# Optimization experiments

Hardware: AMD Instinct MI355X
Metric: run time of the kernel (lower is better)

The kernel has to match this reference:

```python
import jax, jax.numpy as jnp
import numpy as np

D_MODEL = 1024
NUM_HEADS = 16
D_K = D_MODEL // NUM_HEADS


def setup_inputs() -> dict:
    key = jax.random.key(0)
    ks = jax.random.split(key, 9)
    s = 1.0 / np.sqrt(D_MODEL)
    x = jax.random.normal(ks[0], (2, 2048, D_MODEL), dtype=jnp.float32)
    mk = lambda k: jax.random.uniform(k, (D_MODEL, D_MODEL), jnp.float32, -s, s)
    mb = lambda k: jax.random.uniform(k, (D_MODEL,), jnp.float32, -s, s)
    return {
        "x": x,
        "Wq": mk(ks[1]), "bq": mb(ks[2]),
        "Wk": mk(ks[3]), "bk": mb(ks[4]),
        "Wv": mk(ks[5]), "bv": mb(ks[6]),
        "Wo": mk(ks[7]), "bo": mb(ks[8]),
    }


def _attn(x, Wq, bq, Wk, bk, Wv, bv, Wo, bo):
    B, S, _ = x.shape
    # torch Linear: y = x @ W.T + b; weights stored [out, in]
    def proj(W, b):
        y = jnp.einsum('bsd,ed->bse', x, W) + b
        return y.reshape(B, S, NUM_HEADS, D_K).transpose(0, 2, 1, 3)  # [B,H,S,Dk]
    Q = proj(Wq, bq)
    K = proj(Wk, bk)
    V = proj(Wv, bv)
    scale = 1.0 / np.sqrt(D_K).astype(np.float32)
    scores = jnp.einsum('bhqd,bhkd->bhqk', Q, K) * scale  # [B,H,S,S]
    # FAITHFUL to source: softmax over dim=1 (the HEAD axis), a quirk of the original code
    attn = jax.nn.softmax(scores, axis=1)
    context = jnp.einsum('bhqk,bhkd->bhqd', attn, V)  # [B,H,S,Dk]
    context = context.transpose(0, 2, 1, 3).reshape(B, S, D_MODEL)
    return jnp.einsum('bsd,ed->bse', context, Wo) + bo


def reference(x, Wq, bq, Wk, bk, Wv, bv, Wo, bo):
    return _attn(x, Wq, bq, Wk, bk, Wv, bv, Wo, bo)
```

## Files before the change

### kernel.cpp

```cpp
#include <hip/hip_runtime.h>


#define D_MODEL 1024
#define NH 16
#define DKH 64
#define SEQ 2048
#define NB 2
#define NTOK (NB * SEQ)
#define OSC 0.180336880f

typedef float f32x4 __attribute__((ext_vector_type(4)));
typedef short bf16x8 __attribute__((ext_vector_type(8)));

static __device__ __forceinline__ unsigned short f2bf(float x) {
    union { float f; unsigned int u; } c; c.f = x;
    unsigned int r = (c.u + 0x7FFFu + ((c.u >> 16) & 1u)) >> 16;
    return (unsigned short)r;
}
static __device__ __forceinline__ unsigned int pack2(float a, float b) {
    return (unsigned int)f2bf(a) | ((unsigned int)f2bf(b) << 16);
}
static __device__ __forceinline__ unsigned int pack2rn(float a, float b) {
    union { float f; unsigned int u; } ca, cb; ca.f = a; cb.f = b;
    return __builtin_amdgcn_perm(cb.u + 0x8000u, ca.u + 0x8000u, 0x07060302u);
}
static __device__ __forceinline__ unsigned int pack2tr(float a, float b) {
    union { float f; unsigned int u; } ca, cb; ca.f = a; cb.f = b;
    return __builtin_amdgcn_perm(cb.u, ca.u, 0x07060302u);
}
static __device__ __forceinline__ float bflo(unsigned int u) {
    union { unsigned int x; float f; } c; c.x = u << 16; return c.f;
}
static __device__ __forceinline__ float bfhi(unsigned int u) {
    union { unsigned int x; float f; } c; c.x = u & 0xFFFF0000u; return c.f;
}
static __device__ __forceinline__ f32x4 mfma16(uint4 a, uint4 b, f32x4 c) {
    return __builtin_amdgcn_mfma_f32_16x16x32_bf16(
        __builtin_bit_cast(bf16x8, a), __builtin_bit_cast(bf16x8, b), c, 0, 0, 0);
}
static __device__ __forceinline__ void gl_lds16(const unsigned short* g, unsigned short* l) {
    __builtin_amdgcn_global_load_lds(
        (const __attribute__((address_space(1))) unsigned int*)g,
        (__attribute__((address_space(3))) unsigned int*)l, 16, 0, 0);
}
static __device__ __forceinline__ int fsw(int row) {
    return (row & 7) ^ ((row >> 2) & 7);
}

__global__ __launch_bounds__(256) void cvt_k(const float* __restrict__ x,
                                             unsigned short* __restrict__ xb)
{
    size_t i = ((size_t)blockIdx.x * 256 + threadIdx.x) * 8;
    float4 a = *(const float4*)(x + i);
    float4 b = *(const float4*)(x + i + 4);
    uint4 p = { pack2(a.x, a.y), pack2(a.z, a.w), pack2(b.x, b.y), pack2(b.z, b.w) };
    *(uint4*)(xb + i) = p;
}

__global__ __launch_bounds__(256) void cvt_w3(
    const float* __restrict__ w0, const float* __restrict__ w1,
    const float* __restrict__ w2, unsigned short* __restrict__ outb)
{
    int sel = blockIdx.x >> 9;
    int blk = blockIdx.x & 511;
    const float* src = (sel == 0) ? w0 : (sel == 1) ? w1 : w2;
    size_t i = ((size_t)blk * 256 + threadIdx.x) * 8;
    float4 a = *(const float4*)(src + i);
    float4 b = *(const float4*)(src + i + 4);
    uint4 p = { pack2(a.x, a.y), pack2(a.z, a.w), pack2(b.x, b.y), pack2(b.z, b.w) };
    *(uint4*)(outb + (size_t)sel * D_MODEL * D_MODEL + i) = p;
}

__global__ __launch_bounds__(256) void gemm_qkv3(
    const unsigned short* __restrict__ A, const unsigned short* __restrict__ Wb3,
    const float* __restrict__ bq, const float* __restrict__ bk,
    const float* __restrict__ bv, unsigned short* __restrict__ Qh,
    unsigned short* __restrict__ Kh, unsigned short* __restrict__ Vt)
{
    __shared__ unsigned short lds[16384];
    unsigned short* lA = lds;
    unsigned short* lB = lds + 8192;
    const int tid = threadIdx.x;
    const int wv = tid >> 6, lane = tid & 63, quad = lane >> 4, lm = lane & 15;
    const int sel = blockIdx.x >> 3;
    const int m0 = blockIdx.y * 128, n0 = (blockIdx.x & 7) * 128;
    const int sub = lane >> 3, chl = (lane & 7) ^ sub;
    const unsigned short* Wb = Wb3 + (size_t)sel * D_MODEL * D_MODEL;
    const float* bias = (sel == 0) ? bq : (sel == 1) ? bk : bv;
    const float osc = (sel == 0) ? OSC : 1.0f;

    f32x4 acc[2][8] = {};

    for (int k0 = 0; k0 < D_MODEL; k0 += 64) {
        __syncthreads();
#pragma unroll
        for (int j = 0; j < 4; ++j) {
            int rbase = wv * 32 + j * 8;
            gl_lds16(A + (size_t)(m0 + rbase + sub) * D_MODEL + k0 + chl * 8,
                     &lA[rbase * 64]);
            gl_lds16(Wb + (size_t)(n0 + rbase + sub) * D_MODEL + k0 + chl * 8,
                     &lB[rbase * 64]);
        }
        __syncthreads();
#pragma unroll
        for (int ks = 0; ks < 2; ++ks) {
            uint4 af[2];
#pragma unroll
            for (int mt = 0; mt < 2; ++mt)
                af[mt] = *(const uint4*)&lA[(wv * 32 + mt * 16 + lm) * 64 +
                                            ((ks * 4 + quad) ^ (lm & 7)) * 8];
#pragma unroll
            for (int nt = 0; nt < 8; ++nt) {
                uint4 bf = *(const uint4*)&lB[(nt * 16 + lm) * 64 +
                                              ((ks * 4 + quad) ^ (lm & 7)) * 8];
                acc[0][nt] = mfma16(af[0], bf, acc[0][nt]);
                acc[1][nt] = mfma16(af[1], bf, acc[1][nt]);
            }
        }
    }

    if (sel < 2) {
        unsigned short* out = (sel == 0) ? Qh : Kh;
#pragma unroll
        for (int nt = 0; nt < 8; ++nt) {
            int n = n0 + nt * 16 + lm;
            float bvv = bias[n];
            int h = n >> 6, d = n & 63;
#pragma unroll
            for (int mt = 0; mt < 2; ++mt)
#pragma unroll
                for (int r = 0; r < 4; ++r) {
                    int m = m0 + wv * 32 + mt * 16 + quad * 4 + r;
                    int b = m >> 11, q = m & 2047;
                    out[((size_t)(b * NH + h) * SEQ + q) * DKH + d] =
                        f2bf((acc[mt][nt][r] + bvv) * osc);
                }
        }
    } else {
        __syncthreads();
        unsigned short* T = lds;
#pragma unroll
        for (int nt = 0; nt < 8; ++nt) {
            float bvv = bias[n0 + nt * 16 + lm];
            int nl = nt * 16 + lm;
#pragma unroll
            for (int mt = 0; mt < 2; ++mt) {
                int ml = wv * 32 + mt * 16 + quad * 4;
                uint2 p = { pack2rn(acc[mt][nt][0] + bvv, acc[mt][nt][1] + bvv),
                            pack2rn(acc[mt][nt][2] + bvv, acc[mt][nt][3] + bvv) };
                *(uint2*)&T[nl * 128 + ml] = p;
            }
        }
        __syncthreads();
        int row = tid >> 1, seg = tid & 1;
        int b = m0 >> 11, s0 = m0 & 2047;
        unsigned short* dst = Vt + ((size_t)(b * D_MODEL) + n0 + row) * SEQ + s0 + seg * 64;
        const unsigned short* src = &T[row * 128 + seg * 64];
#pragma unroll
        for (int i = 0; i < 8; ++i)
            *(uint4*)(dst + i * 8) = *(const uint4*)(src + i * 8);
    }
}

template <int KS>
__global__ __launch_bounds__(256) void psum(const unsigned short* __restrict__ OP,
                                            unsigned short* __restrict__ OPs)
{
    const size_t M = (size_t)NTOK * D_MODEL;
    size_t i = ((size_t)blockIdx.x * 256 + threadIdx.x) * 8;
    uint4 a = *(const uint4*)(OP + i);
    float lo0 = bflo(a.x), hi0 = bfhi(a.x), lo1 = bflo(a.y), hi1 = bfhi(a.y);
    float lo2 = bflo(a.z), hi2 = bfhi(a.z), lo3 = bflo(a.w), hi3 = bfhi(a.w);
#pragma unroll
    for (int p = 1; p < KS; ++p) {
        uint4 u = *(const uint4*)(OP + p * M + i);
        lo0 += bflo(u.x); hi0 += bfhi(u.x); lo1 += bflo(u.y); hi1 += bfhi(u.y);
        lo2 += bflo(u.z); hi2 += bfhi(u.z); lo3 += bflo(u.w); hi3 += bfhi(u.w);
    }
    uint4 o = { pack2(lo0, hi0), pack2(lo1, hi1), pack2(lo2, hi2), pack2(lo3, hi3) };
    *(uint4*)(OPs + i) = o;
}

__global__ __launch_bounds__(256) void gemm_osum1(
    const unsigned short* __restrict__ OPs, const unsigned short* __restrict__ WoB,
    const float* __restrict__ bias, float* __restrict__ out)
{
    __shared__ unsigned short lds[16384];
    unsigned short* lA = lds;
    unsigned short* lB = lds + 8192;
    const int tid = threadIdx.x;
    const int wv = tid >> 6, lane = tid & 63, quad = lane >> 4, lm = lane & 15;
    const int m0 = blockIdx.y * 128, n0 = blockIdx.x * 128;
    const int sub = lane >> 3, chl = (lane & 7) ^ sub;
    const int b = m0 >> 11, q0 = m0 & 2047;

    f32x4 acc[2][8] = {};

    for (int k0 = 0; k0 < D_MODEL; k0 += 64) {
        const int h = k0 >> 6;
        const unsigned short* Ab = OPs + ((size_t)(b * NH + h) * SEQ + q0) * DKH;
        __syncthreads();
#pragma unroll
        for (int j = 0; j < 4; ++j) {
            int rbase = wv * 32 + j * 8;
            gl_lds16(Ab + (size_t)(rbase + sub) * DKH + chl * 8, &lA[rbase * 64]);
            gl_lds16(WoB + (size_t)(n0 + rbase + sub) * D_MODEL + k0 + chl * 8,
                     &lB[rbase * 64]);
        }
        __syncthreads();
#pragma unroll
        for (int ks = 0; ks < 2; ++ks) {
            uint4 af[2];
#pragma unroll
            for (int mt = 0; mt < 2; ++mt)
                af[mt] = *(const uint4*)&lA[(wv * 32 + mt * 16 + lm) * 64 +
                                            ((ks * 4 + quad) ^ (lm & 7)) * 8];
#pragma unroll
            for (int nt = 0; nt < 8; ++nt) {
                uint4 bf = *(const uint4*)&lB[(nt * 16 + lm) * 64 +
                                              ((ks * 4 + quad) ^ (lm & 7)) * 8];
                acc[0][nt] = mfma16(af[0], bf, acc[0][nt]);
                acc[1][nt] = mfma16(af[1], bf, acc[1][nt]);
            }
        }
    }
#pragma unroll
    for (int nt = 0; nt < 8; ++nt) {
        int n = n0 + nt * 16 + lm;
        float bv = bias[n];
#pragma unroll
        for (int mt = 0; mt < 2; ++mt)
#pragma unroll
            for (int r = 0; r < 4; ++r) {
                int m = m0 + wv * 32 + mt * 16 + quad * 4 + r;
                out[(size_t)m * D_MODEL + n] = acc[mt][nt][r] + bv;
            }
    }
}

__global__ __launch_bounds__(256) void zker2(
    const unsigned short* __restrict__ Qh, const unsigned short* __restrict__ Kh,
    unsigned short* __restrict__ rz)
{
    __shared__ unsigned short lK[128 * 64];
    const int tid = threadIdx.x;
    const int wv = tid >> 6, lane = tid & 63, quad = lane >> 4, lm = lane & 15;
    const int lid = blockIdx.x;
    const int xcd = lid & 7, slot = lid >> 3;
    const int qb = slot & 15, col = xcd * 4 + (slot >> 4);
    const int b = col >> 4, kb = col & 15;
    const int q0 = qb * 128, k0 = kb * 128;
    const int srow = tid >> 3, sc = tid & 7;

    f32x4 z[2][8] = {};

    for (int h = 0; h < NH; ++h) {
        const size_t kbase = ((size_t)(b * NH + h) * SEQ + k0) * DKH;
        __syncthreads();
#pragma unroll
        for (int j = 0; j < 4; ++j) {
            int row = j * 32 + srow;
            int g = sc ^ fsw(row);
            gl_lds16(Kh + kbase + (size_t)row * 64 + g * 8, &lK[(j * 32 + wv * 8) * 64]);
        }
        uint4 bq[2][2];
#pragma unroll
        for (int qs = 0; qs < 2; ++qs) {
            const unsigned short* qp = Qh +
                ((size_t)(b * NH + h) * SEQ + q0 + wv * 32 + qs * 16 + lm) * DKH + quad * 8;
            bq[qs][0] = *(const uint4*)qp;
            bq[qs][1] = *(const uint4*)(qp + 32);
        }
        __syncthreads();
#pragma unroll
        for (int kt = 0; kt < 8; ++kt) {
            int krow = kt * 16 + lm;
            uint4 a0 = *(const uint4*)&lK[krow * 64 + ((quad) ^ fsw(krow)) * 8];
            uint4 a1 = *(const uint4*)&lK[krow * 64 + ((4 + quad) ^ fsw(krow)) * 8];
#pragma unroll
            for (int qs = 0; qs < 2; ++qs) {
                f32x4 sf = {0.f, 0.f, 0.f, 0.f};
                sf = mfma16(a0, bq[qs][0], sf);
                sf = mfma16(a1, bq[qs][1], sf);
#pragma unroll
                for (int r = 0; r < 4; ++r)
                    z[qs][kt][r] += __builtin_amdgcn_exp2f(sf[r]);
            }
        }
    }
#pragma unroll
    for (int qs = 0; qs < 2; ++qs) {
        int q = q0 + wv * 32 + qs * 16 + lm;
#pragma unroll
        for (int kt = 0; kt < 8; ++kt) {
            int k = k0 + kt * 16 + quad * 4;
            float l0 = __builtin_amdgcn_logf(z[qs][kt][0]);
            float l1 = __builtin_amdgcn_logf(z[qs][kt][1]);
            float l2 = __builtin_amdgcn_logf(z[qs][kt][2]);
            float l3 = __builtin_amdgcn_logf(z[qs][kt][3]);
            uint2 st = { pack2rn(-l0, -l1), pack2rn(-l2, -l3) };
            *(uint2*)(rz + (size_t)(b * SEQ + q) * SEQ + k) = st;
        }
    }
}

template <int KS>
__global__ __launch_bounds__(256) void attn4(
    const unsigned short* __restrict__ Qh, const unsigned short* __restrict__ Kh,
    const unsigned short* __restrict__ Vt, const unsigned short* __restrict__ rz,
    unsigned short* __restrict__ OP)
{
    __shared__ unsigned short lK[64 * 64];
    __shared__ unsigned short lV[64 * 64];
    const int tid = threadIdx.x;
    const int wv = tid >> 6, lane = tid & 63, quad = lane >> 4, lm = lane & 15;
    const int lid = blockIdx.x;
    const int xcd = lid & 7, slot = lid >> 3;
    const int qb = slot & 15;
    const int combo = xcd * (4 * KS) + (slot >> 4);
    const int bh = combo / KS, ksl = combo % KS;
    const int b = bh >> 4, h = bh & 15;
    const int q0 = qb * 128;
    const int NIT = (SEQ / KS) / 64;
    const int kbeg = ksl * (SEQ / KS);
    const int q0w = q0 + wv * 32;
    const size_t hb = (size_t)(b * NH + h) * SEQ;
    const int srow = tid >> 3, sc = tid & 7;

    uint4 qf[2][2];
#pragma unroll
    for (int qs = 0; qs < 2; ++qs)
#pragma unroll
        for (int ks = 0; ks < 2; ++ks)
            qf[qs][ks] = *(const uint4*)(Qh + (hb + q0w + qs * 16 + lm) * DKH +
                                         ks * 32 + quad * 8);

    const int perm = ((lm >> 2) * 8) + (lm & 3);
    f32x4 oa[4][2] = {};

    for (int kt = 0; kt < NIT; ++kt) {
        const int kbase = kbeg + kt * 64;
        __syncthreads();
#pragma unroll
        for (int j = 0; j < 2; ++j) {
            int row = j * 32 + srow;
            int g = sc ^ fsw(row);
            gl_lds16(Kh + (hb + kbase + row) * DKH + g * 8,
                     &lK[(j * 32 + wv * 8) * 64]);
        }
#pragma unroll
        for (int j = 0; j < 2; ++j) {
            int row = j * 32 + srow;
            int g = sc ^ fsw(row);
            gl_lds16(Vt + ((size_t)(b * D_MODEL) + h * DKH + row) * SEQ + kbase + g * 8,
                     &lV[(j * 32 + wv * 8) * 64]);
        }
        uint4 rv[2][2];
#pragma unroll
        for (int qs = 0; qs < 2; ++qs)
#pragma unroll
            for (int gr = 0; gr < 2; ++gr)
                rv[gr][qs] = *(const uint4*)(rz +
                    (size_t)(b * SEQ + q0w + qs * 16 + lm) * SEQ +
                    kbase + gr * 32 + quad * 8);
        __syncthreads();

#pragma unroll
        for (int gr = 0; gr < 2; ++gr) {
            f32x4 sf[2][2];
#pragma unroll
            for (int qs = 0; qs < 2; ++qs) {
                uint4 rq = rv[gr][qs];
                sf[0][qs][0] = bflo(rq.x); sf[0][qs][1] = bfhi(rq.x);
                sf[0][qs][2] = bflo(rq.y); sf[0][qs][3] = bfhi(rq.y);
                sf[1][qs][0] = bflo(rq.z); sf[1][qs][1] = bfhi(rq.z);
                sf[1][qs][2] = bflo(rq.w); sf[1][qs][3] = bfhi(rq.w);
            }
#pragma unroll
            for (int sel = 0; sel < 2; ++sel) {
                int key = gr * 32 + perm + sel * 4;
#pragma unroll
                for (int ks = 0; ks < 2; ++ks) {
                    uint4 kfv = *(const uint4*)&lK[key * 64 +
                                                   ((ks * 4 + quad) ^ fsw(key)) * 8];
                    sf[sel][0] = mfma16(kfv, qf[0][ks], sf[sel][0]);
                    sf[sel][1] = mfma16(kfv, qf[1][ks], sf[sel][1]);
                }
            }
            uint4 pk[2];
#pragma unroll
            for (int qs = 0; qs < 2; ++qs) {
                float p00 = __builtin_amdgcn_exp2f(sf[0][qs][0]);
                float p01 = __builtin_amdgcn_exp2f(sf[0][qs][1]);
                float p02 = __builtin_amdgcn_exp2f(sf[0][qs][2]);
                float p03 = __builtin_amdgcn_exp2f(sf[0][qs][3]);
                float p10 = __builtin_amdgcn_exp2f(sf[1][qs][0]);
                float p11 = __builtin_amdgcn_exp2f(sf[1][qs][1]);
                float p12 = __builtin_amdgcn_exp2f(sf[1][qs][2]);
                float p13 = __builtin_amdgcn_exp2f(sf[1][qs][3]);
                pk[qs].x = pack2tr(p00, p01);
                pk[qs].y = pack2tr(p02, p03);
                pk[qs].z = pack2tr(p10, p11);
                pk[qs].w = pack2tr(p12, p13);
            }
#pragma unroll
            for (int ct = 0; ct < 4; ++ct) {
                int vrow = ct * 16 + lm;
                uint4 vfv = *(const uint4*)&lV[vrow * 64 +
                                               ((gr * 4 + quad) ^ fsw(vrow)) * 8];
                oa[ct][0] = mfma16(vfv, pk[0], oa[ct][0]);
                oa[ct][1] = mfma16(vfv, pk[1], oa[ct][1]);
            }
        }
    }

    unsigned short* op = OP + (size_t)ksl * NTOK * D_MODEL;
#pragma unroll
    for (int ct = 0; ct < 4; ++ct)
#pragma unroll
        for (int qs = 0; qs < 2; ++qs) {
            uint2 st = { pack2rn(oa[ct][qs][0], oa[ct][qs][1]),
                         pack2rn(oa[ct][qs][2], oa[ct][qs][3]) };
            *(uint2*)(op + (hb + q0w + qs * 16 + lm) * DKH + ct * 16 + quad * 4) = st;
        }
}

extern "C" void kernel_launch(void* const* d_in, const int* in_sizes, int n_in,
                              void* d_out, int out_size, void* d_ws, size_t ws_size,
                              hipStream_t stream)
{
    const float* x  = (const float*)d_in[0];
    const float* Wq = (const float*)d_in[1];
    const float* bq = (const float*)d_in[2];
    const float* Wk = (const float*)d_in[3];
    const float* bk = (const float*)d_in[4];
    const float* Wv = (const float*)d_in[5];
    const float* bv = (const float*)d_in[6];
    const float* Wo = (const float*)d_in[7];
    const float* bo = (const float*)d_in[8];
    float* out = (float*)d_out;

    const size_t M  = (size_t)NTOK * D_MODEL;
    const size_t RZ = (size_t)NB * SEQ * SEQ;
    unsigned short* ws = (unsigned short*)d_ws;
    unsigned short* rzb = ws;
    unsigned short* xb  = ws;
    unsigned short* Qh  = ws + RZ;
    unsigned short* Kh  = Qh + M;
    unsigned short* Vt  = Kh + M;
    unsigned short* OP  = Vt + M;
    unsigned short* Wb3 = OP;
    unsigned short* OPs = Qh;
    unsigned short* WoB = rzb;

    const size_t need4 = (RZ + 3 * M + 4 * M) * sizeof(unsigned short);
    const size_t need2 = (RZ + 3 * M + 2 * M) * sizeof(unsigned short);
    const int KS = (ws_size >= need4) ? 4 : (ws_size >= need2) ? 2 : 1;

    cvt_k<<<2048, 256, 0, stream>>>(x, xb);
    cvt_w3<<<1536, 256, 0, stream>>>(Wq, Wk, Wv, Wb3);
    gemm_qkv3<<<dim3(24, 32), 256, 0, stream>>>(xb, Wb3, bq, bk, bv, Qh, Kh, Vt);
    zker2<<<512, 256, 0, stream>>>(Qh, Kh, rzb);
    if (KS == 4)      attn4<4><<<2048, 256, 0, stream>>>(Qh, Kh, Vt, rzb, OP);
    else if (KS == 2) attn4<2><<<1024, 256, 0, stream>>>(Qh, Kh, Vt, rzb, OP);
    else              attn4<1><<<512, 256, 0, stream>>>(Qh, Kh, Vt, rzb, OP);
    cvt_k<<<512, 256, 0, stream>>>(Wo, WoB);
    if (KS == 4)      psum<4><<<2048, 256, 0, stream>>>(OP, OPs);
    else if (KS == 2) psum<2><<<2048, 256, 0, stream>>>(OP, OPs);
    else              OPs = OP;
    gemm_osum1<<<dim3(8, 32), 256, 0, stream>>>(OPs, WoB, bo, out);
}
```

Baseline: 268.6 us.

## Double-buffer K/V LDS staging and prefetch next tile in score and attention kernels

Both the log-normaliser kernel (zker2) and the attention kernel (attn4) now use two LDS buffers. The next head's or next key tile's K/V is issued into the alternate buffer before computing on the current one, and the Q fragments and rz rows are prefetched into registers the same way. This leaves one barrier per iteration instead of two and is meant to hide global-load latency behind the MFMA and exp work. s_setprio is raised around the MFMA sequences to favour matrix issue. The cost is doubled LDS per block and extra live registers for the prefetched fragments, which may lower occupancy.

```diff
diff --git a/kernel.cpp b/kernel.cpp
--- a/kernel.cpp
+++ b/kernel.cpp
@@ -242,7 +242,7 @@
     const unsigned short* __restrict__ Qh, const unsigned short* __restrict__ Kh,
     unsigned short* __restrict__ rz)
 {
-    __shared__ unsigned short lK[128 * 64];
+    __shared__ unsigned short lK[2][128 * 64];
     const int tid = threadIdx.x;
     const int wv = tid >> 6, lane = tid & 63, quad = lane >> 4, lm = lane & 15;
     const int lid = blockIdx.x;
@@ -254,37 +254,62 @@
 
     f32x4 z[2][8] = {};
 
-    for (int h = 0; h < NH; ++h) {
-        const size_t kbase = ((size_t)(b * NH + h) * SEQ + k0) * DKH;
-        __syncthreads();
+    auto stagek = [&](int buf, int hh) {
+        const size_t kbase = ((size_t)(b * NH + hh) * SEQ + k0) * DKH;
 #pragma unroll
         for (int j = 0; j < 4; ++j) {
             int row = j * 32 + srow;
             int g = sc ^ fsw(row);
-            gl_lds16(Kh + kbase + (size_t)row * 64 + g * 8, &lK[(j * 32 + wv * 8) * 64]);
-        }
-        uint4 bq[2][2];
+            gl_lds16(Kh + kbase + (size_t)row * 64 + g * 8,
+                     &lK[buf][(j * 32 + wv * 8) * 64]);
+        }
+    };
+    auto loadq = [&](uint4 (&bqr)[2][2], int hh) {
 #pragma unroll
         for (int qs = 0; qs < 2; ++qs) {
             const unsigned short* qp = Qh +
-                ((size_t)(b * NH + h) * SEQ + q0 + wv * 32 + qs * 16 + lm) * DKH + quad * 8;
-            bq[qs][0] = *(const uint4*)qp;
-            bq[qs][1] = *(const uint4*)(qp + 32);
-        }
-        __syncthreads();
+                ((size_t)(b * NH + hh) * SEQ + q0 + wv * 32 + qs * 16 + lm) * DKH + quad * 8;
+            bqr[qs][0] = *(const uint4*)qp;
+            bqr[qs][1] = *(const uint4*)(qp + 32);
+        }
+    };
+
+    uint4 bq[2][2];
+    stagek(0, 0);
+    loadq(bq, 0);
+    __syncthreads();
+
+    for (int h = 0; h < NH; ++h) {
+        const int cur = h & 1;
+        uint4 bqn[2][2];
+        if (h + 1 < NH) {
+            stagek(cur ^ 1, h + 1);
+            loadq(bqn, h + 1);
+        }
+        const unsigned short* cK = lK[cur];
 #pragma unroll
         for (int kt = 0; kt < 8; ++kt) {
             int krow = kt * 16 + lm;
-            uint4 a0 = *(const uint4*)&lK[krow * 64 + ((quad) ^ fsw(krow)) * 8];
-            uint4 a1 = *(const uint4*)&lK[krow * 64 + ((4 + quad) ^ fsw(krow)) * 8];
+            uint4 a0 = *(const uint4*)&cK[krow * 64 + ((quad) ^ fsw(krow)) * 8];
+            uint4 a1 = *(const uint4*)&cK[krow * 64 + ((4 + quad) ^ fsw(krow)) * 8];
 #pragma unroll
             for (int qs = 0; qs < 2; ++qs) {
                 f32x4 sf = {0.f, 0.f, 0.f, 0.f};
+                __builtin_amdgcn_s_setprio(1);
                 sf = mfma16(a0, bq[qs][0], sf);
                 sf = mfma16(a1, bq[qs][1], sf);
+                __builtin_amdgcn_s_setprio(0);
 #pragma unroll
                 for (int r = 0; r < 4; ++r)
                     z[qs][kt][r] += __builtin_amdgcn_exp2f(sf[r]);
+            }
+        }
+        __syncthreads();
+        if (h + 1 < NH) {
+#pragma unroll
+            for (int qs = 0; qs < 2; ++qs) {
+                bq[qs][0] = bqn[qs][0];
+                bq[qs][1] = bqn[qs][1];
             }
         }
     }
@@ -310,8 +335,8 @@
     const unsigned short* __restrict__ Vt, const unsigned short* __restrict__ rz,
     unsigned short* __restrict__ OP)
 {
-    __shared__ unsigned short lK[64 * 64];
-    __shared__ unsigned short lV[64 * 64];
+    __shared__ unsigned short lK[2][64 * 64];
+    __shared__ unsigned short lV[2][64 * 64];
     const int tid = threadIdx.x;
     const int wv = tid >> 6, lane = tid & 63, quad = lane >> 4, lm = lane & 15;
     const int lid = blockIdx.x;
@@ -335,35 +360,50 @@
             qf[qs][ks] = *(const uint4*)(Qh + (hb + q0w + qs * 16 + lm) * DKH +
                                          ks * 32 + quad * 8);
 
-    const int perm = ((lm >> 2) * 8) + (lm & 3);
-    f32x4 oa[4][2] = {};
-
-    for (int kt = 0; kt < NIT; ++kt) {
-        const int kbase = kbeg + kt * 64;
-        __syncthreads();
+    auto stage = [&](int buf, int kb2) {
 #pragma unroll
         for (int j = 0; j < 2; ++j) {
             int row = j * 32 + srow;
             int g = sc ^ fsw(row);
-            gl_lds16(Kh + (hb + kbase + row) * DKH + g * 8,
-                     &lK[(j * 32 + wv * 8) * 64]);
+            gl_lds16(Kh + (hb + kb2 + row) * DKH + g * 8,
+                     &lK[buf][(j * 32 + wv * 8) * 64]);
         }
 #pragma unroll
         for (int j = 0; j < 2; ++j) {
             int row = j * 32 + srow;
             int g = sc ^ fsw(row);
-            gl_lds16(Vt + ((size_t)(b * D_MODEL) + h * DKH + row) * SEQ + kbase + g * 8,
-                     &lV[(j * 32 + wv * 8) * 64]);
-        }
-        uint4 rv[2][2];
+            gl_lds16(Vt + ((size_t)(b * D_MODEL) + h * DKH + row) * SEQ + kb2 + g * 8,
+                     &lV[buf][(j * 32 + wv * 8) * 64]);
+        }
+    };
+    auto loadrv = [&](uint4 (&r)[2][2], int kb2) {
 #pragma unroll
         for (int qs = 0; qs < 2; ++qs)
 #pragma unroll
             for (int gr = 0; gr < 2; ++gr)
-                rv[gr][qs] = *(const uint4*)(rz +
+                r[gr][qs] = *(const uint4*)(rz +
                     (size_t)(b * SEQ + q0w + qs * 16 + lm) * SEQ +
-                    kbase + gr * 32 + quad * 8);
-        __syncthreads();
+                    kb2 + gr * 32 + quad * 8);
+    };
+
+    const int perm = ((lm >> 2) * 8) + (lm & 3);
+    f32x4 oa[4][2] = {};
+
+    uint4 rv[2][2];
+    stage(0, kbeg);
+    loadrv(rv, kbeg);
+    __syncthreads();
+
+    for (int kt = 0; kt < NIT; ++kt) {
+        const int cur = kt & 1;
+        const int kbase = kbeg + kt * 64;
+        uint4 rvn[2][2];
+        if (kt + 1 < NIT) {
+            stage(cur ^ 1, kbase + 64);
+            loadrv(rvn, kbase + 64);
+        }
+        const unsigned short* cK = lK[cur];
+        const unsigned short* cV = lV[cur];
 
 #pragma unroll
         for (int gr = 0; gr < 2; ++gr) {
@@ -376,17 +416,19 @@
                 sf[1][qs][0] = bflo(rq.z); sf[1][qs][1] = bfhi(rq.z);
                 sf[1][qs][2] = bflo(rq.w); sf[1][qs][3] = bfhi(rq.w);
             }
+            __builtin_amdgcn_s_setprio(1);
 #pragma unroll
             for (int sel = 0; sel < 2; ++sel) {
                 int key = gr * 32 + perm + sel * 4;
 #pragma unroll
                 for (int ks = 0; ks < 2; ++ks) {
-                    uint4 kfv = *(const uint4*)&lK[key * 64 +
+                    uint4 kfv = *(const uint4*)&cK[key * 64 +
                                                    ((ks * 4 + quad) ^ fsw(key)) * 8];
                     sf[sel][0] = mfma16(kfv, qf[0][ks], sf[sel][0]);
                     sf[sel][1] = mfma16(kfv, qf[1][ks], sf[sel][1]);
                 }
             }
+            __builtin_amdgcn_s_setprio(0);
             uint4 pk[2];
 #pragma unroll
             for (int qs = 0; qs < 2; ++qs) {
@@ -403,14 +445,24 @@
                 pk[qs].z = pack2tr(p10, p11);
                 pk[qs].w = pack2tr(p12, p13);
             }
+            __builtin_amdgcn_s_setprio(1);
 #pragma unroll
             for (int ct = 0; ct < 4; ++ct) {
                 int vrow = ct * 16 + lm;
-                uint4 vfv = *(const uint4*)&lV[vrow * 64 +
+                uint4 vfv = *(const uint4*)&cV[vrow * 64 +
                                                ((gr * 4 + quad) ^ fsw(vrow)) * 8];
                 oa[ct][0] = mfma16(vfv, pk[0], oa[ct][0]);
                 oa[ct][1] = mfma16(vfv, pk[1], oa[ct][1]);
             }
+            __builtin_amdgcn_s_setprio(0);
+        }
+        __syncthreads();
+        if (kt + 1 < NIT) {
+#pragma unroll
+            for (int a = 0; a < 2; ++a)
+#pragma unroll
+                for (int c = 0; c < 2; ++c)
+                    rv[a][c] = rvn[a][c];
         }
     }
 
```

Result: no change. 272.2 us (+1.3%).
